# Kernel optimization log

Measured on AMD Instinct MI355X. Metric: run time of the kernel, lower is better.

Reference implementation:

```python
import jax, jax.numpy as jnp
import numpy as np
from jax import lax

B, T, V, E, H2, S, C = 64, 2048, 4096, 128, 128, 8, 2
H = 2 * H2  # lstm_dim


def _run_lstm(x, lens, W_ih, W_hh, b, reverse):
    """Single-direction LSTM over padded [B,T,E] with valid lengths lens.
    Masked steps (t >= len) leave the carry unchanged; PyTorch gate order i,f,g,o."""
    Bn, Tn, _ = x.shape
    xg = jnp.einsum('bte,ge->btg', x, W_ih) + b  # [B,T,4*H2] precomputed input gates
    ts = jnp.arange(Tn)

    def step(carry, inp):
        h, c = carry
        xt, t = inp
        g = xt + h @ W_hh.T
        i, f, gg, o = jnp.split(g, 4, axis=-1)
        c_new = jax.nn.sigmoid(f) * c + jax.nn.sigmoid(i) * jnp.tanh(gg)
        h_new = jax.nn.sigmoid(o) * jnp.tanh(c_new)
        m = (t < lens)[:, None]
        h = jnp.where(m, h_new, h)
        c = jnp.where(m, c_new, c)
        return (h, c), h

    init = (jnp.zeros((Bn, H2), x.dtype), jnp.zeros((Bn, H2), x.dtype))
    _, hs = lax.scan(step, init, (jnp.swapaxes(xg, 0, 1), ts), reverse=reverse)
    return jnp.swapaxes(hs, 0, 1)  # [B,T,H2]


def _seg_maxpool(h, lens):
    """Ragged dynamic max-pool: per sample, window=ceil(L/S), zero-pad to window*S,
    max over each window -> [B,S,H]. Matches take_max/max_every_k_seg."""
    Bn, Tn, Hc = h.shape
    NEG = jnp.finfo(h.dtype).min
    w = (lens + S - 1) // S  # per-sample window [B]
    t = jnp.arange(Tn)
    seg = jnp.minimum(t[None, :] // w[:, None], S - 1)        # [B,T]
    valid = t[None, :] < lens[:, None]                        # [B,T]
    ids = jnp.where(valid, seg + S * jnp.arange(Bn)[:, None], Bn * S)
    vals = jnp.where(valid[:, :, None], h, NEG)
    m = jax.ops.segment_max(vals.reshape(Bn * Tn, Hc), ids.reshape(-1),
                            num_segments=Bn * S + 1)[:Bn * S].reshape(Bn, S, Hc)
    # segments overlapping the zero-padded tail [L, w*S) include value 0
    has_pad = (jnp.arange(S)[None, :] >= lens[:, None] // w[:, None]) & \
              (w[:, None] * S > lens[:, None])
    pad_floor = jnp.where(has_pad, jnp.zeros((), h.dtype), NEG)
    return jnp.maximum(m, pad_floor[:, :, None])


def setup_inputs() -> dict:
    key = jax.random.key(0)
    ks = jax.random.split(key, 11)
    sentence = jax.random.randint(ks[0], (B, T), 0, V, dtype=jnp.int32)
    lens = jax.random.randint(ks[1], (B,), T // 2, T + 1, dtype=jnp.int32)
    seq_lengths = jnp.sort(lens)[::-1]  # descending, as pack_padded_sequence requires
    s = 0.05
    return {
        'sentence': sentence,
        'seq_lengths': seq_lengths,
        'emb': jax.random.normal(ks[2], (V, E), jnp.float32) * s,
        'W_ih_f': jax.random.normal(ks[3], (4 * H2, E), jnp.float32) * s,
        'W_hh_f': jax.random.normal(ks[4], (4 * H2, H2), jnp.float32) * s,
        'b_f': jax.random.normal(ks[5], (4 * H2,), jnp.float32) * s,
        'W_ih_b': jax.random.normal(ks[6], (4 * H2, E), jnp.float32) * s,
        'W_hh_b': jax.random.normal(ks[7], (4 * H2, H2), jnp.float32) * s,
        'b_b': jax.random.normal(ks[8], (4 * H2,), jnp.float32) * s,
        'W_dense': jax.random.normal(ks[9], (C, H * S), jnp.float32) * s,
        'b_dense': jax.random.normal(ks[10], (C,), jnp.float32) * s,
    }


def reference(sentence, seq_lengths, emb, W_ih_f, W_hh_f, b_f,
              W_ih_b, W_hh_b, b_b, W_dense, b_dense):
    x = emb[sentence]                                          # [B,T,E]
    hf = _run_lstm(x, seq_lengths, W_ih_f, W_hh_f, b_f, False)
    hb = _run_lstm(x, seq_lengths, W_ih_b, W_hh_b, b_b, True)
    h = jnp.concatenate([hf, hb], axis=-1)                     # [B,T,H]
    pooled = _seg_maxpool(h, seq_lengths)                      # [B,S,H]
    flat = jnp.swapaxes(pooled, 1, 2).reshape(pooled.shape[0], H * S)  # (hidden, segment) order
    return flat @ W_dense.T + b_dense                          # [B,C]
```

## Files before the change

kernel.cpp:

```cpp
#include <hip/hip_runtime.h>
#include <hip/hip_bf16.h>
#include <math.h>

#define BB 64
#define TT 2048
#define VV 4096
#define EE 128
#define H2 128
#define SS 8
#define CC 2

typedef _Float16 h2f __attribute__((ext_vector_type(2)));

__device__ __forceinline__ float fast_rcp(float x) {
#if __has_builtin(__builtin_amdgcn_rcpf)
    return __builtin_amdgcn_rcpf(x);
#else
    return 1.f / x;
#endif
}

__device__ __forceinline__ float sigf(float x) {
    return fast_rcp(1.f + __expf(-x));
}
__device__ __forceinline__ float tanh_fast(float x) {
    return fmaf(-2.f, fast_rcp(__expf(2.f * x) + 1.f), 1.f);
}

__device__ __forceinline__ float dot2acc(h2f w, h2f h, float acc) {
#if __has_builtin(__builtin_amdgcn_fdot2)
    return __builtin_amdgcn_fdot2(w, h, acc, false);
#else
    return fmaf((float)w.x, (float)h.x, fmaf((float)w.y, (float)h.y, acc));
#endif
}

__device__ __forceinline__ float xor1_swap(float x) {
#if __has_builtin(__builtin_amdgcn_update_dpp)
    return __builtin_bit_cast(float,
        __builtin_amdgcn_update_dpp(0, __builtin_bit_cast(int, x),
                                    0xB1, 0xF, 0xF, true));
#else
    return __shfl_xor(x, 1, 64);
#endif
}

__device__ __forceinline__ void lds_barrier() {
    asm volatile("s_waitcnt lgkmcnt(0)" ::: "memory");
    __builtin_amdgcn_s_barrier();
    asm volatile("" ::: "memory");
}

__global__ __launch_bounds__(256) void eg_gemm(
    const float* __restrict__ emb,
    const float* __restrict__ Wf, const float* __restrict__ bf,
    const float* __restrict__ Wb, const float* __restrict__ bb,
    float* __restrict__ EGp)
{
    __shared__ float As[64][68];
    __shared__ float Bs[64][68];

    const int tid = threadIdx.x;
    const int tx = tid & 15, ty = tid >> 4;
    const int m0 = blockIdx.y * 64;
    const int n0 = blockIdx.x * 64;

    const float* Bsrc;
    const float* bias;
    if (n0 < 512) { Bsrc = Wf + n0 * EE; bias = bf + n0; }
    else          { Bsrc = Wb + (n0 - 512) * EE; bias = bb + (n0 - 512); }

    float acc[4][4] = {};

    for (int kc = 0; kc < 2; ++kc) {
        for (int c = tid; c < 1024; c += 256) {
            int r = c >> 4, q = c & 15;
            float4 av = *(const float4*)(emb + (size_t)(m0 + r) * EE + kc * 64 + q * 4);
            As[q * 4 + 0][r] = av.x; As[q * 4 + 1][r] = av.y;
            As[q * 4 + 2][r] = av.z; As[q * 4 + 3][r] = av.w;
            float4 bv = *(const float4*)(Bsrc + (size_t)r * EE + kc * 64 + q * 4);
            Bs[q * 4 + 0][r] = bv.x; Bs[q * 4 + 1][r] = bv.y;
            Bs[q * 4 + 2][r] = bv.z; Bs[q * 4 + 3][r] = bv.w;
        }
        __syncthreads();
        #pragma unroll 8
        for (int k = 0; k < 64; ++k) {
            float4 a4 = *(const float4*)&As[k][4 * ty];
            float4 b4 = *(const float4*)&Bs[k][4 * tx];
            float a[4] = {a4.x, a4.y, a4.z, a4.w};
            float b[4] = {b4.x, b4.y, b4.z, b4.w};
            #pragma unroll
            for (int i = 0; i < 4; ++i)
                #pragma unroll
                for (int jn = 0; jn < 4; ++jn)
                    acc[i][jn] = fmaf(a[i], b[jn], acc[i][jn]);
        }
        __syncthreads();
    }

    #pragma unroll
    for (int i = 0; i < 4; ++i) {
        int m = m0 + 4 * ty + i;
        #pragma unroll
        for (int jn = 0; jn < 4; ++jn) {
            int nn = 4 * tx + jn;
            int n = n0 + nn;
            int d = n >> 9;
            int r = n & 511;
            int slot = (r >> 7) & 1;
            int p = (r & 127) + (r >= 256 ? 128 : 0);
            EGp[(((size_t)m * 2 + d) * 256 + p) * 2 + slot] = acc[i][jn] + bias[nn];
        }
    }
}


#define LSTM_STEP(T_, BUF_, XV_, TOKN_, ISSUE_)                              \
  {                                                                          \
    float2 xv_ = (XV_);                  \
    if (ISSUE_) {                                                            \
      (XV_) = egp[((size_t)(TOKN_) * 2 + dir) * 256 + p];      \
      int i4_ = dir ? (L - 5 - (T_)) : ((T_) + 4);             \
      i4_ = max(0, min(TT - 1, i4_));                                        \
      (TOKN_) = srow[i4_];                                                   \
    }                                                                        \
    float a00 = 0.f, a01 = 0.f, a10 = 0.f, a11 = 0.f;                       \
    _Pragma("unroll")                                                        \
    for (int k4 = 0; k4 < 16; ++k4) {                                        \
      int4 hc = *(const int4*)&hpk[BUF_][4 * k4];        \
      h2f hv0 = __builtin_bit_cast(h2f, hc.x);                               \
      h2f hv1 = __builtin_bit_cast(h2f, hc.y);                               \
      h2f hv2 = __builtin_bit_cast(h2f, hc.z);                               \
      h2f hv3 = __builtin_bit_cast(h2f, hc.w);                               \
      a00 = dot2acc(w0[4 * k4 + 0], hv0, a00);                               \
      a10 = dot2acc(w1[4 * k4 + 0], hv0, a10);                               \
      a01 = dot2acc(w0[4 * k4 + 1], hv1, a01);                               \
      a11 = dot2acc(w1[4 * k4 + 1], hv1, a11);                               \
      a00 = dot2acc(w0[4 * k4 + 2], hv2, a00);                               \
      a10 = dot2acc(w1[4 * k4 + 2], hv2, a10);                               \
      a01 = dot2acc(w0[4 * k4 + 3], hv3, a01);                               \
      a11 = dot2acc(w1[4 * k4 + 3], hv3, a11);                               \
    }                                                                        \
    float g0 = (a00 + a01) + xv_.x;      \
    float g1 = (a10 + a11) + xv_.y;      \
    float s_own = sigf(g1);                                     \
    float t_own = evn ? sigf(g0) : tanh_fast(g0);               \
    float t_x = xor1_swap(t_own);                                            \
    float s_x = xor1_swap(s_own);                                            \
    c = s_own * c + t_own * t_x;                                             \
    float hn = s_x * tanh_fast(c);                                           \
    const int tt_ = dir ? (L - 1 - (T_)) : (T_);                             \
    bool bnd_ = dir ? (tt_ < nb) : (tt_ >= nb);                              \
    if (bnd_) {                                                              \
      if (evn) {                                                             \
        float v = pm;                                                        \
        if (haspad && cur_seg >= padlo) v = fmaxf(v, 0.f);                   \
        pws[(((size_t)b * 2 + dir) * SS + cur_seg) * H2 + u] = v;            \
      }                                                                      \
      pm = -INFINITY;                                                        \
      cur_seg += dir ? -1 : 1;                                               \
      nb += dir ? -wseg : wseg;                                              \
    }                                                                        \
    pm = fmaxf(pm, hn);                                                      \
    if (evn) ((_Float16*)hpk[(BUF_) ^ 1])[u] = (_Float16)hn;                 \
    lds_barrier();                                                           \
  }

__global__ __launch_bounds__(256, 1) void lstm_rec(
    const int* __restrict__ sentence, const int* __restrict__ lens,
    const float* __restrict__ Whhf, const float* __restrict__ Whhb,
    const float* __restrict__ EGp, float* __restrict__ pws)
{
    const int bid = blockIdx.x;
    const int b = bid >> 1;
    const int dir = bid & 1;
    const int tid = threadIdx.x;
    const int l = tid & 63;
    const int wv = tid >> 6;
    const int u = wv * 32 + (l >> 1);
    const bool evn = (l & 1) == 0;
    const int L = lens[b];
    const int* __restrict__ srow = sentence + (size_t)b * TT;

    const int r0 = evn ? u : (256 + u);
    const int r1 = r0 + 128;
    const float* __restrict__ Wh = (dir == 0 ? Whhf : Whhb);

    h2f w0[64], w1[64];
    #pragma unroll
    for (int k4 = 0; k4 < 32; ++k4) {
        float4 a = *(const float4*)(Wh + (size_t)r0 * H2 + 4 * k4);
        w0[2 * k4 + 0].x = (_Float16)a.x; w0[2 * k4 + 0].y = (_Float16)a.y;
        w0[2 * k4 + 1].x = (_Float16)a.z; w0[2 * k4 + 1].y = (_Float16)a.w;
        float4 bq = *(const float4*)(Wh + (size_t)r1 * H2 + 4 * k4);
        w1[2 * k4 + 0].x = (_Float16)bq.x; w1[2 * k4 + 0].y = (_Float16)bq.y;
        w1[2 * k4 + 1].x = (_Float16)bq.z; w1[2 * k4 + 1].y = (_Float16)bq.w;
    }

    __shared__ __align__(16) int hpk[2][64];
    if (tid < 64) hpk[0][tid] = 0;

    const int p = evn ? u : (128 + u);
    const float2* __restrict__ egp = (const float2*)EGp;

    float c = 0.f;
    float pm = -INFINITY;

    const int wseg = (L + SS - 1) >> 3;
    const bool haspad = (SS * wseg > L);
    const int padlo = L / wseg;
    int cur_seg = dir ? (SS - 1) : 0;
    int nb = dir ? (SS - 1) * wseg : wseg;

    float2 e0, e1;
    int tokA, tokB;
    {
        int j0 = dir ? (L - 1) : 0;
        e0 = egp[((size_t)srow[j0] * 2 + dir) * 256 + p];
        int j1 = dir ? (L - 2) : 1;  j1 = max(0, min(TT - 1, j1));
        e1 = egp[((size_t)srow[j1] * 2 + dir) * 256 + p];
        int j2 = dir ? (L - 3) : 2;  j2 = max(0, min(TT - 1, j2));
        tokA = srow[j2];
        int j3 = dir ? (L - 4) : 3;  j3 = max(0, min(TT - 1, j3));
        tokB = srow[j3];
    }

    __syncthreads();

    int t = 0;
    for (; t + 2 <= L; t += 2) {
        LSTM_STEP(t,     0, e0, tokA, true);
        LSTM_STEP(t + 1, 1, e1, tokB, true);
    }
    if (t < L) {
        LSTM_STEP(t, 0, e0, tokA, false);
    }

    if (evn) {
        float v = pm;
        if (haspad && cur_seg >= padlo) v = fmaxf(v, 0.f);
        pws[(((size_t)b * 2 + dir) * SS + cur_seg) * H2 + u] = v;
    }
}

__global__ __launch_bounds__(256) void dense_k(
    const float* __restrict__ pws, const float* __restrict__ Wd,
    const float* __restrict__ bd, float* __restrict__ out)
{
    const int b = blockIdx.x;
    const int tid = threadIdx.x;
    float a0 = 0.f, a1 = 0.f;
    for (int k = tid; k < 2048; k += 256) {
        int h = k >> 3, s = k & 7;
        int dir = h >> 7, j = h & 127;
        float v = pws[(((size_t)b * 2 + dir) * SS + s) * H2 + j];
        a0 = fmaf(v, Wd[k], a0);
        a1 = fmaf(v, Wd[2048 + k], a1);
    }
    __shared__ float r0[256], r1[256];
    r0[tid] = a0; r1[tid] = a1;
    __syncthreads();
    for (int s = 128; s > 0; s >>= 1) {
        if (tid < s) { r0[tid] += r0[tid + s]; r1[tid] += r1[tid + s]; }
        __syncthreads();
    }
    if (tid == 0) {
        out[b * 2 + 0] = r0[0] + bd[0];
        out[b * 2 + 1] = r1[0] + bd[1];
    }
}

extern "C" void kernel_launch(void* const* d_in, const int* in_sizes, int n_in,
                              void* d_out, int out_size, void* d_ws, size_t ws_size,
                              hipStream_t stream)
{
    const int*   sentence = (const int*)d_in[0];
    const int*   lens     = (const int*)d_in[1];
    const float* emb      = (const float*)d_in[2];
    const float* Wihf     = (const float*)d_in[3];
    const float* Whhf     = (const float*)d_in[4];
    const float* bf       = (const float*)d_in[5];
    const float* Wihb     = (const float*)d_in[6];
    const float* Whhb     = (const float*)d_in[7];
    const float* bb       = (const float*)d_in[8];
    const float* Wd       = (const float*)d_in[9];
    const float* bd       = (const float*)d_in[10];
    float* out = (float*)d_out;

    float* EGp = (float*)d_ws;
    float* pws = EGp + (size_t)VV * 1024;

    eg_gemm<<<dim3(16, 64), 256, 0, stream>>>(emb, Wihf, bf, Wihb, bb, EGp);
    lstm_rec<<<128, 256, 0, stream>>>(sentence, lens, Whhf, Whhb, EGp, pws);
    dense_k<<<64, 256, 0, stream>>>(pws, Wd, bd, out);
}
```

Baseline: 1.268 ms.

## Fuse forward and backward LSTM directions into one block per sample

Each block now runs both LSTM directions for one batch sample, interleaving the two independent recurrences in one step with a shared barrier, so the grid shrinks from 128 to 64 blocks. The goal is to hide the serial latency of each step (LDS reads, dot products, transcendentals, barrier) by giving each wave two independent dependency chains, and to halve the barrier count per direction-step. In exchange each thread holds 256 packed-half weight registers instead of 128, which risks spills, and only 64 CUs are occupied.

```diff
diff --git a/kernel.cpp b/kernel.cpp
--- a/kernel.cpp
+++ b/kernel.cpp
@@ -115,54 +115,102 @@
 }
 
 
-#define LSTM_STEP(T_, BUF_, XV_, TOKN_, ISSUE_)                              \
+#define STEP_BOTH(T_, BUF_, XVF_, XVB_, TKF_, TKB_, ISSUE_)                  \
   {                                                                          \
-    float2 xv_ = (XV_);                  \
+    float2 xvf_ = (XVF_);                \
+    float2 xvb_ = (XVB_);                                                    \
     if (ISSUE_) {                                                            \
-      (XV_) = egp[((size_t)(TOKN_) * 2 + dir) * 256 + p];      \
-      int i4_ = dir ? (L - 5 - (T_)) : ((T_) + 4);             \
-      i4_ = max(0, min(TT - 1, i4_));                                        \
-      (TOKN_) = srow[i4_];                                                   \
-    }                                                                        \
-    float a00 = 0.f, a01 = 0.f, a10 = 0.f, a11 = 0.f;                       \
+      (XVF_) = egp[((size_t)(TKF_) * 2 + 0) * 256 + p];        \
+      (XVB_) = egp[((size_t)(TKB_) * 2 + 1) * 256 + p];                      \
+      int i4f_ = max(0, min(TT - 1, (T_) + 4));                \
+      (TKF_) = srow[i4f_];                                                   \
+      int i4b_ = max(0, min(TT - 1, L - 5 - (T_)));                          \
+      (TKB_) = srow[i4b_];                                                   \
+    }                                                                        \
+    float a00f = 0.f, a01f = 0.f, a10f = 0.f, a11f = 0.f;                    \
+    float a00b = 0.f, a01b = 0.f, a10b = 0.f, a11b = 0.f;                    \
     _Pragma("unroll")                                                        \
     for (int k4 = 0; k4 < 16; ++k4) {                                        \
-      int4 hc = *(const int4*)&hpk[BUF_][4 * k4];        \
-      h2f hv0 = __builtin_bit_cast(h2f, hc.x);                               \
-      h2f hv1 = __builtin_bit_cast(h2f, hc.y);                               \
-      h2f hv2 = __builtin_bit_cast(h2f, hc.z);                               \
-      h2f hv3 = __builtin_bit_cast(h2f, hc.w);                               \
-      a00 = dot2acc(w0[4 * k4 + 0], hv0, a00);                               \
-      a10 = dot2acc(w1[4 * k4 + 0], hv0, a10);                               \
-      a01 = dot2acc(w0[4 * k4 + 1], hv1, a01);                               \
-      a11 = dot2acc(w1[4 * k4 + 1], hv1, a11);                               \
-      a00 = dot2acc(w0[4 * k4 + 2], hv2, a00);                               \
-      a10 = dot2acc(w1[4 * k4 + 2], hv2, a10);                               \
-      a01 = dot2acc(w0[4 * k4 + 3], hv3, a01);                               \
-      a11 = dot2acc(w1[4 * k4 + 3], hv3, a11);                               \
-    }                                                                        \
-    float g0 = (a00 + a01) + xv_.x;      \
-    float g1 = (a10 + a11) + xv_.y;      \
-    float s_own = sigf(g1);                                     \
-    float t_own = evn ? sigf(g0) : tanh_fast(g0);               \
-    float t_x = xor1_swap(t_own);                                            \
-    float s_x = xor1_swap(s_own);                                            \
-    c = s_own * c + t_own * t_x;                                             \
-    float hn = s_x * tanh_fast(c);                                           \
-    const int tt_ = dir ? (L - 1 - (T_)) : (T_);                             \
-    bool bnd_ = dir ? (tt_ < nb) : (tt_ >= nb);                              \
-    if (bnd_) {                                                              \
-      if (evn) {                                                             \
-        float v = pm;                                                        \
-        if (haspad && cur_seg >= padlo) v = fmaxf(v, 0.f);                   \
-        pws[(((size_t)b * 2 + dir) * SS + cur_seg) * H2 + u] = v;            \
+      int4 hcf = *(const int4*)&hpkF[BUF_][4 * k4];      \
+      int4 hcb = *(const int4*)&hpkB[BUF_][4 * k4];                          \
+      h2f f0 = __builtin_bit_cast(h2f, hcf.x);                               \
+      h2f f1 = __builtin_bit_cast(h2f, hcf.y);                               \
+      h2f f2 = __builtin_bit_cast(h2f, hcf.z);                               \
+      h2f f3 = __builtin_bit_cast(h2f, hcf.w);                               \
+      h2f b0 = __builtin_bit_cast(h2f, hcb.x);                               \
+      h2f b1 = __builtin_bit_cast(h2f, hcb.y);                               \
+      h2f b2 = __builtin_bit_cast(h2f, hcb.z);                               \
+      h2f b3 = __builtin_bit_cast(h2f, hcb.w);                               \
+      a00f = dot2acc(w0f[4 * k4 + 0], f0, a00f);                             \
+      a00b = dot2acc(w0b[4 * k4 + 0], b0, a00b);                             \
+      a10f = dot2acc(w1f[4 * k4 + 0], f0, a10f);                             \
+      a10b = dot2acc(w1b[4 * k4 + 0], b0, a10b);                             \
+      a01f = dot2acc(w0f[4 * k4 + 1], f1, a01f);                             \
+      a01b = dot2acc(w0b[4 * k4 + 1], b1, a01b);                             \
+      a11f = dot2acc(w1f[4 * k4 + 1], f1, a11f);                             \
+      a11b = dot2acc(w1b[4 * k4 + 1], b1, a11b);                             \
+      a00f = dot2acc(w0f[4 * k4 + 2], f2, a00f);                             \
+      a00b = dot2acc(w0b[4 * k4 + 2], b2, a00b);                             \
+      a10f = dot2acc(w1f[4 * k4 + 2], f2, a10f);                             \
+      a10b = dot2acc(w1b[4 * k4 + 2], b2, a10b);                             \
+      a01f = dot2acc(w0f[4 * k4 + 3], f3, a01f);                             \
+      a01b = dot2acc(w0b[4 * k4 + 3], b3, a01b);                             \
+      a11f = dot2acc(w1f[4 * k4 + 3], f3, a11f);                             \
+      a11b = dot2acc(w1b[4 * k4 + 3], b3, a11b);                             \
+    }                                                                        \
+                                                      \
+    float g0f = (a00f + a01f) + xvf_.x;                                      \
+    float g1f = (a10f + a11f) + xvf_.y;                                      \
+    float sof = sigf(g1f);                                                   \
+    float tof = evn ? sigf(g0f) : tanh_fast(g0f);                            \
+        \
+    float g0b = (a00b + a01b) + xvb_.x;                                      \
+    float g1b = (a10b + a11b) + xvb_.y;                                      \
+    float sob = sigf(g1b);                                                   \
+    float tob = evn ? sigf(g0b) : tanh_fast(g0b);                            \
+    float txf = xor1_swap(tof);                                              \
+    float sxf = xor1_swap(sof);                                              \
+    float txb = xor1_swap(tob);                                              \
+    float sxb = xor1_swap(sob);                                              \
+    cf = sof * cf + tof * txf;                                               \
+    cb = sob * cb + tob * txb;                                               \
+    float hnf = sxf * tanh_fast(cf);                                         \
+    float hnb = sxb * tanh_fast(cb);                                         \
+                                                    \
+    {                                                                        \
+      bool bnd_ = ((T_) >= nbf);                                             \
+      if (bnd_) {                                                            \
+        if (evn) {                                                           \
+          float v = pmf;                                                     \
+          if (haspad && cur_segf >= padlo) v = fmaxf(v, 0.f);                \
+          pws[(((size_t)b * 2 + 0) * SS + cur_segf) * H2 + u] = v;           \
+        }                                                                    \
+        pmf = -INFINITY;                                                     \
+        cur_segf += 1;                                                       \
+        nbf += wseg;                                                         \
       }                                                                      \
-      pm = -INFINITY;                                                        \
-      cur_seg += dir ? -1 : 1;                                               \
-      nb += dir ? -wseg : wseg;                                              \
-    }                                                                        \
-    pm = fmaxf(pm, hn);                                                      \
-    if (evn) ((_Float16*)hpk[(BUF_) ^ 1])[u] = (_Float16)hn;                 \
+      pmf = fmaxf(pmf, hnf);                                                 \
+    }                                                                        \
+                                                    \
+    {                                                                        \
+      const int ttb_ = L - 1 - (T_);                                         \
+      bool bnd_ = (ttb_ < nbb);                                              \
+      if (bnd_) {                                                            \
+        if (evn) {                                                           \
+          float v = pmb;                                                     \
+          if (haspad && cur_segb >= padlo) v = fmaxf(v, 0.f);                \
+          pws[(((size_t)b * 2 + 1) * SS + cur_segb) * H2 + u] = v;           \
+        }                                                                    \
+        pmb = -INFINITY;                                                     \
+        cur_segb -= 1;                                                       \
+        nbb -= wseg;                                                         \
+      }                                                                      \
+      pmb = fmaxf(pmb, hnb);                                                 \
+    }                                                                        \
+    if (evn) {                                                               \
+      ((_Float16*)hpkF[(BUF_) ^ 1])[u] = (_Float16)hnf;                      \
+      ((_Float16*)hpkB[(BUF_) ^ 1])[u] = (_Float16)hnb;                      \
+    }                                                                        \
     lds_barrier();                                                           \
   }
 
@@ -171,9 +219,7 @@
     const float* __restrict__ Whhf, const float* __restrict__ Whhb,
     const float* __restrict__ EGp, float* __restrict__ pws)
 {
-    const int bid = blockIdx.x;
-    const int b = bid >> 1;
-    const int dir = bid & 1;
+    const int b = blockIdx.x;
     const int tid = threadIdx.x;
     const int l = tid & 63;
     const int wv = tid >> 6;
@@ -184,62 +230,76 @@
 
     const int r0 = evn ? u : (256 + u);
     const int r1 = r0 + 128;
-    const float* __restrict__ Wh = (dir == 0 ? Whhf : Whhb);
-
-    h2f w0[64], w1[64];
+
+    h2f w0f[64], w1f[64], w0b[64], w1b[64];
     #pragma unroll
     for (int k4 = 0; k4 < 32; ++k4) {
-        float4 a = *(const float4*)(Wh + (size_t)r0 * H2 + 4 * k4);
-        w0[2 * k4 + 0].x = (_Float16)a.x; w0[2 * k4 + 0].y = (_Float16)a.y;
-        w0[2 * k4 + 1].x = (_Float16)a.z; w0[2 * k4 + 1].y = (_Float16)a.w;
-        float4 bq = *(const float4*)(Wh + (size_t)r1 * H2 + 4 * k4);
-        w1[2 * k4 + 0].x = (_Float16)bq.x; w1[2 * k4 + 0].y = (_Float16)bq.y;
-        w1[2 * k4 + 1].x = (_Float16)bq.z; w1[2 * k4 + 1].y = (_Float16)bq.w;
-    }
-
-    __shared__ __align__(16) int hpk[2][64];
-    if (tid < 64) hpk[0][tid] = 0;
+        float4 a = *(const float4*)(Whhf + (size_t)r0 * H2 + 4 * k4);
+        w0f[2 * k4 + 0].x = (_Float16)a.x; w0f[2 * k4 + 0].y = (_Float16)a.y;
+        w0f[2 * k4 + 1].x = (_Float16)a.z; w0f[2 * k4 + 1].y = (_Float16)a.w;
+        float4 bq = *(const float4*)(Whhf + (size_t)r1 * H2 + 4 * k4);
+        w1f[2 * k4 + 0].x = (_Float16)bq.x; w1f[2 * k4 + 0].y = (_Float16)bq.y;
+        w1f[2 * k4 + 1].x = (_Float16)bq.z; w1f[2 * k4 + 1].y = (_Float16)bq.w;
+        float4 c4 = *(const float4*)(Whhb + (size_t)r0 * H2 + 4 * k4);
+        w0b[2 * k4 + 0].x = (_Float16)c4.x; w0b[2 * k4 + 0].y = (_Float16)c4.y;
+        w0b[2 * k4 + 1].x = (_Float16)c4.z; w0b[2 * k4 + 1].y = (_Float16)c4.w;
+        float4 d4 = *(const float4*)(Whhb + (size_t)r1 * H2 + 4 * k4);
+        w1b[2 * k4 + 0].x = (_Float16)d4.x; w1b[2 * k4 + 0].y = (_Float16)d4.y;
+        w1b[2 * k4 + 1].x = (_Float16)d4.z; w1b[2 * k4 + 1].y = (_Float16)d4.w;
+    }
+
+    __shared__ __align__(16) int hpk[2][2][64];
+    int (*hpkF)[64] = hpk[0];
+    int (*hpkB)[64] = hpk[1];
+    if (tid < 128) hpk[tid >> 6][0][tid & 63] = 0;
 
     const int p = evn ? u : (128 + u);
     const float2* __restrict__ egp = (const float2*)EGp;
 
-    float c = 0.f;
-    float pm = -INFINITY;
+    float cf = 0.f, cb = 0.f;
+    float pmf = -INFINITY, pmb = -INFINITY;
 
     const int wseg = (L + SS - 1) >> 3;
     const bool haspad = (SS * wseg > L);
     const int padlo = L / wseg;
-    int cur_seg = dir ? (SS - 1) : 0;
-    int nb = dir ? (SS - 1) * wseg : wseg;
-
-    float2 e0, e1;
-    int tokA, tokB;
+    int cur_segf = 0,      nbf = wseg;
+    int cur_segb = SS - 1, nbb = (SS - 1) * wseg;
+
+    float2 e0f, e1f, e0b, e1b;
+    int tokAf, tokBf, tokAb, tokBb;
     {
-        int j0 = dir ? (L - 1) : 0;
-        e0 = egp[((size_t)srow[j0] * 2 + dir) * 256 + p];
-        int j1 = dir ? (L - 2) : 1;  j1 = max(0, min(TT - 1, j1));
-        e1 = egp[((size_t)srow[j1] * 2 + dir) * 256 + p];
-        int j2 = dir ? (L - 3) : 2;  j2 = max(0, min(TT - 1, j2));
-        tokA = srow[j2];
-        int j3 = dir ? (L - 4) : 3;  j3 = max(0, min(TT - 1, j3));
-        tokB = srow[j3];
+        e0f = egp[((size_t)srow[0] * 2 + 0) * 256 + p];
+        int j1 = min(TT - 1, 1);
+        e1f = egp[((size_t)srow[j1] * 2 + 0) * 256 + p];
+        tokAf = srow[max(0, min(TT - 1, 2))];
+        tokBf = srow[max(0, min(TT - 1, 3))];
+
+        int j0b = L - 1;
+        e0b = egp[((size_t)srow[j0b] * 2 + 1) * 256 + p];
+        int j1b = max(0, L - 2);
+        e1b = egp[((size_t)srow[j1b] * 2 + 1) * 256 + p];
+        tokAb = srow[max(0, L - 3)];
+        tokBb = srow[max(0, L - 4)];
     }
 
     __syncthreads();
 
     int t = 0;
     for (; t + 2 <= L; t += 2) {
-        LSTM_STEP(t,     0, e0, tokA, true);
-        LSTM_STEP(t + 1, 1, e1, tokB, true);
+        STEP_BOTH(t,     0, e0f, e0b, tokAf, tokAb, true);
+        STEP_BOTH(t + 1, 1, e1f, e1b, tokBf, tokBb, true);
     }
     if (t < L) {
-        LSTM_STEP(t, 0, e0, tokA, false);
+        STEP_BOTH(t, 0, e0f, e0b, tokAf, tokAb, false);
     }
 
     if (evn) {
-        float v = pm;
-        if (haspad && cur_seg >= padlo) v = fmaxf(v, 0.f);
-        pws[(((size_t)b * 2 + dir) * SS + cur_seg) * H2 + u] = v;
+        float v = pmf;
+        if (haspad && cur_segf >= padlo) v = fmaxf(v, 0.f);
+        pws[(((size_t)b * 2 + 0) * SS + cur_segf) * H2 + u] = v;
+        v = pmb;
+        if (haspad && cur_segb >= padlo) v = fmaxf(v, 0.f);
+        pws[(((size_t)b * 2 + 1) * SS + cur_segb) * H2 + u] = v;
     }
 }
 
@@ -291,6 +351,6 @@
     float* pws = EGp + (size_t)VV * 1024;
 
     eg_gemm<<<dim3(16, 64), 256, 0, stream>>>(emb, Wihf, bf, Wihb, bb, EGp);
-    lstm_rec<<<128, 256, 0, stream>>>(sentence, lens, Whhf, Whhb, EGp, pws);
+    lstm_rec<<<64, 256, 0, stream>>>(sentence, lens, Whhf, Whhb, EGp, pws);
     dense_k<<<64, 256, 0, stream>>>(pws, Wd, bd, out);
 }
```

After: 2.585 ms. +103.9%, slower.

## Split LSTM recurrent matvec along K across lane pairs instead of gates

Applied to the files above, without the earlier changes.

Each lane pair previously split the four gate rows (each lane computing two full 128-length dot products). Now each lane computes partial dot products for all four gates over half of the hidden dimension (64 elements), and the pair combines the halves with cross-lane swaps before the activations. This halves the LDS reads of h per lane, using four independent accumulator chains per half for more ILP. The cost is four extra cross-lane swaps and adds per step. The store of the new h into LDS is also moved earlier, ahead of the segment-boundary pooling logic.

```diff
diff --git a/kernel.cpp b/kernel.cpp
--- a/kernel.cpp
+++ b/kernel.cpp
@@ -124,31 +124,72 @@
       i4_ = max(0, min(TT - 1, i4_));                                        \
       (TOKN_) = srow[i4_];                                                   \
     }                                                                        \
-    float a00 = 0.f, a01 = 0.f, a10 = 0.f, a11 = 0.f;                       \
+    float c0a = 0.f, c1a = 0.f, c2a = 0.f, c3a = 0.f;                        \
+    float c0b = 0.f, c1b = 0.f, c2b = 0.f, c3b = 0.f;                        \
+    const int4* hb4 = (const int4*)&hpk[BUF_][hoff];                         \
     _Pragma("unroll")                                                        \
-    for (int k4 = 0; k4 < 16; ++k4) {                                        \
-      int4 hc = *(const int4*)&hpk[BUF_][4 * k4];        \
-      h2f hv0 = __builtin_bit_cast(h2f, hc.x);                               \
-      h2f hv1 = __builtin_bit_cast(h2f, hc.y);                               \
-      h2f hv2 = __builtin_bit_cast(h2f, hc.z);                               \
-      h2f hv3 = __builtin_bit_cast(h2f, hc.w);                               \
-      a00 = dot2acc(w0[4 * k4 + 0], hv0, a00);                               \
-      a10 = dot2acc(w1[4 * k4 + 0], hv0, a10);                               \
-      a01 = dot2acc(w0[4 * k4 + 1], hv1, a01);                               \
-      a11 = dot2acc(w1[4 * k4 + 1], hv1, a11);                               \
-      a00 = dot2acc(w0[4 * k4 + 2], hv2, a00);                               \
-      a10 = dot2acc(w1[4 * k4 + 2], hv2, a10);                               \
-      a01 = dot2acc(w0[4 * k4 + 3], hv3, a01);                               \
-      a11 = dot2acc(w1[4 * k4 + 3], hv3, a11);                               \
+    for (int k8 = 0; k8 < 8; k8 += 2) {                                      \
+      int4 u0 = hb4[k8];                                                     \
+      int4 u1 = hb4[k8 + 1];                                                 \
+      h2f h0 = __builtin_bit_cast(h2f, u0.x);                                \
+      h2f h1 = __builtin_bit_cast(h2f, u0.y);                                \
+      h2f h2 = __builtin_bit_cast(h2f, u0.z);                                \
+      h2f h3 = __builtin_bit_cast(h2f, u0.w);                                \
+      h2f h4 = __builtin_bit_cast(h2f, u1.x);                                \
+      h2f h5 = __builtin_bit_cast(h2f, u1.y);                                \
+      h2f h6 = __builtin_bit_cast(h2f, u1.z);                                \
+      h2f h7 = __builtin_bit_cast(h2f, u1.w);                                \
+      c0a = dot2acc(wg[0][4 * k8 + 0], h0, c0a);                             \
+      c1a = dot2acc(wg[1][4 * k8 + 0], h0, c1a);                             \
+      c2a = dot2acc(wg[2][4 * k8 + 0], h0, c2a);                             \
+      c3a = dot2acc(wg[3][4 * k8 + 0], h0, c3a);                             \
+      c0b = dot2acc(wg[0][4 * k8 + 4], h4, c0b);                             \
+      c1b = dot2acc(wg[1][4 * k8 + 4], h4, c1b);                             \
+      c2b = dot2acc(wg[2][4 * k8 + 4], h4, c2b);                             \
+      c3b = dot2acc(wg[3][4 * k8 + 4], h4, c3b);                             \
+      c0a = dot2acc(wg[0][4 * k8 + 1], h1, c0a);                             \
+      c1a = dot2acc(wg[1][4 * k8 + 1], h1, c1a);                             \
+      c2a = dot2acc(wg[2][4 * k8 + 1], h1, c2a);                             \
+      c3a = dot2acc(wg[3][4 * k8 + 1], h1, c3a);                             \
+      c0b = dot2acc(wg[0][4 * k8 + 5], h5, c0b);                             \
+      c1b = dot2acc(wg[1][4 * k8 + 5], h5, c1b);                             \
+      c2b = dot2acc(wg[2][4 * k8 + 5], h5, c2b);                             \
+      c3b = dot2acc(wg[3][4 * k8 + 5], h5, c3b);                             \
+      c0a = dot2acc(wg[0][4 * k8 + 2], h2, c0a);                             \
+      c1a = dot2acc(wg[1][4 * k8 + 2], h2, c1a);                             \
+      c2a = dot2acc(wg[2][4 * k8 + 2], h2, c2a);                             \
+      c3a = dot2acc(wg[3][4 * k8 + 2], h2, c3a);                             \
+      c0b = dot2acc(wg[0][4 * k8 + 6], h6, c0b);                             \
+      c1b = dot2acc(wg[1][4 * k8 + 6], h6, c1b);                             \
+      c2b = dot2acc(wg[2][4 * k8 + 6], h6, c2b);                             \
+      c3b = dot2acc(wg[3][4 * k8 + 6], h6, c3b);                             \
+      c0a = dot2acc(wg[0][4 * k8 + 3], h3, c0a);                             \
+      c1a = dot2acc(wg[1][4 * k8 + 3], h3, c1a);                             \
+      c2a = dot2acc(wg[2][4 * k8 + 3], h3, c2a);                             \
+      c3a = dot2acc(wg[3][4 * k8 + 3], h3, c3a);                             \
+      c0b = dot2acc(wg[0][4 * k8 + 7], h7, c0b);                             \
+      c1b = dot2acc(wg[1][4 * k8 + 7], h7, c1b);                             \
+      c2b = dot2acc(wg[2][4 * k8 + 7], h7, c2b);                             \
+      c3b = dot2acc(wg[3][4 * k8 + 7], h7, c3b);                             \
     }                                                                        \
-    float g0 = (a00 + a01) + xv_.x;      \
-    float g1 = (a10 + a11) + xv_.y;      \
+    float o0 = c0a + c0b;                 \
+    float o1 = c1a + c1b;                              \
+    float o2 = c2a + c2b;                              \
+    float o3 = c3a + c3b;                              \
+    float x0 = xor1_swap(o0);                                                \
+    float x1 = xor1_swap(o1);                                                \
+    float x2 = xor1_swap(o2);                                                \
+    float x3 = xor1_swap(o3);                                                \
+    float g0 = (evn ? (o0 + x0) : (o2 + x2)) + xv_.x;      \
+    float g1 = (evn ? (o1 + x1) : (o3 + x3)) + xv_.y;      \
     float s_own = sigf(g1);                                     \
     float t_own = evn ? sigf(g0) : tanh_fast(g0);               \
     float t_x = xor1_swap(t_own);                                            \
     float s_x = xor1_swap(s_own);                                            \
     c = s_own * c + t_own * t_x;                                             \
     float hn = s_x * tanh_fast(c);                                           \
+             \
+    if (evn) ((_Float16*)hpk[(BUF_) ^ 1])[u] = (_Float16)hn;                 \
     const int tt_ = dir ? (L - 1 - (T_)) : (T_);                             \
     bool bnd_ = dir ? (tt_ < nb) : (tt_ >= nb);                              \
     if (bnd_) {                                                              \
@@ -162,7 +203,6 @@
       nb += dir ? -wseg : wseg;                                              \
     }                                                                        \
     pm = fmaxf(pm, hn);                                                      \
-    if (evn) ((_Float16*)hpk[(BUF_) ^ 1])[u] = (_Float16)hn;                 \
     lds_barrier();                                                           \
   }
 
@@ -181,20 +221,23 @@
     const bool evn = (l & 1) == 0;
     const int L = lens[b];
     const int* __restrict__ srow = sentence + (size_t)b * TT;
-
-    const int r0 = evn ? u : (256 + u);
-    const int r1 = r0 + 128;
     const float* __restrict__ Wh = (dir == 0 ? Whhf : Whhb);
 
-    h2f w0[64], w1[64];
+    const int kb = evn ? 0 : 64;
+    const int hoff = evn ? 0 : 32;
+
+    h2f wg[4][32];
     #pragma unroll
-    for (int k4 = 0; k4 < 32; ++k4) {
-        float4 a = *(const float4*)(Wh + (size_t)r0 * H2 + 4 * k4);
-        w0[2 * k4 + 0].x = (_Float16)a.x; w0[2 * k4 + 0].y = (_Float16)a.y;
-        w0[2 * k4 + 1].x = (_Float16)a.z; w0[2 * k4 + 1].y = (_Float16)a.w;
-        float4 bq = *(const float4*)(Wh + (size_t)r1 * H2 + 4 * k4);
-        w1[2 * k4 + 0].x = (_Float16)bq.x; w1[2 * k4 + 0].y = (_Float16)bq.y;
-        w1[2 * k4 + 1].x = (_Float16)bq.z; w1[2 * k4 + 1].y = (_Float16)bq.w;
+    for (int g = 0; g < 4; ++g) {
+        const float* src = Wh + (size_t)(g * 128 + u) * H2 + kb;
+        #pragma unroll
+        for (int k4 = 0; k4 < 16; ++k4) {
+            float4 a = *(const float4*)(src + 4 * k4);
+            wg[g][2 * k4 + 0].x = (_Float16)a.x;
+            wg[g][2 * k4 + 0].y = (_Float16)a.y;
+            wg[g][2 * k4 + 1].x = (_Float16)a.z;
+            wg[g][2 * k4 + 1].y = (_Float16)a.w;
+        }
     }
 
     __shared__ __align__(16) int hpk[2][64];
```

Result: faster. 1.225 ms (-3.4%).
